# Performance work log

Hardware: AMD Instinct MI355X
Metric: run time of the kernel (lower is better)

## Reference

```python
import jax, jax.numpy as jnp
import numpy as np

NV, NC, E, H, L = 100_000, 420_000, 630_000, 128, 8
ALPHA, THETA = 0.1, 0.5


def _seg_mean(msgs, dst, n_dst):
    # mean aggregation over destination segments (PyG SAGEConv default)
    s = jax.ops.segment_sum(msgs, dst, num_segments=n_dst)
    cnt = jax.ops.segment_sum(jnp.ones((dst.shape[0], 1), msgs.dtype), dst, num_segments=n_dst)
    return s / jnp.maximum(cnt, 1.0)


def _sage(x_src, x_dst, src, dst, n_dst, Wl, bl, Wr):
    # SAGEConv: lin_l(mean_{j in N(i)} x_j) + lin_r(x_i); lin_r has no bias
    agg = _seg_mean(x_src[src], dst, n_dst)
    return agg @ Wl + bl + x_dst @ Wr


def setup_inputs() -> dict:
    key = jax.random.key(0)
    ks = jax.random.split(key, 40)
    k = iter(range(40))
    rn = lambda shape, s=0.05: jax.random.normal(ks[next(k)], shape, jnp.float32) * s
    inp = {}
    inp['x_variable'] = jax.random.normal(ks[next(k)], (NV, 4), jnp.float32)
    inp['x_clause'] = jax.random.normal(ks[next(k)], (NC, 1), jnp.float32)
    src_p = jax.random.randint(ks[next(k)], (E,), 0, NV)
    dst_p = jax.random.randint(ks[next(k)], (E,), 0, NC)
    src_n = jax.random.randint(ks[next(k)], (E,), 0, NV)
    dst_n = jax.random.randint(ks[next(k)], (E,), 0, NC)
    inp['edge_pos'] = jnp.stack([src_p, dst_p])  # variable -> clause
    inp['edge_neg'] = jnp.stack([src_n, dst_n])
    inp['W_vemb'] = rn((4, H)); inp['b_vemb'] = rn((H,))
    inp['W_cemb'] = rn((1, H)); inp['b_cemb'] = rn((H,))
    for tag in ('pos', 'neg', 'rpos', 'rneg'):
        inp[f'Wl_{tag}'] = rn((L, H, H)); inp[f'bl_{tag}'] = rn((L, H))
        inp[f'Wr_{tag}'] = rn((L, H, H))
    inp['Wv'] = rn((L, H, H)); inp['bv'] = rn((L, H))
    inp['W_fin'] = rn((H, 1)); inp['b_fin'] = rn((1,))
    return inp


def reference(x_variable, x_clause, edge_pos, edge_neg,
              W_vemb, b_vemb, W_cemb, b_cemb,
              Wl_pos, bl_pos, Wr_pos, Wl_neg, bl_neg, Wr_neg,
              Wl_rpos, bl_rpos, Wr_rpos, Wl_rneg, bl_rneg, Wr_rneg,
              Wv, bv, W_fin, b_fin):
    v_h0 = jax.nn.relu(x_variable @ W_vemb + b_vemb)
    c_h0 = jax.nn.relu(x_clause @ W_cemb + b_cemb)
    v_h, c_h = v_h0, c_h0
    sp, dp = edge_pos[0], edge_pos[1]
    sn, dn = edge_neg[0], edge_neg[1]
    for i in range(L):
        v_old = v_h
        # HeteroConv(aggr='sum'): clause gets pos_in + neg_in, variable gets rev_pos_in + rev_neg_in
        c_new = (_sage(v_h, c_h, sp, dp, NC, Wl_pos[i], bl_pos[i], Wr_pos[i]) +
                 _sage(v_h, c_h, sn, dn, NC, Wl_neg[i], bl_neg[i], Wr_neg[i]))
        v_new = (_sage(c_h, v_h, dp, sp, NV, Wl_rpos[i], bl_rpos[i], Wr_rpos[i]) +
                 _sage(c_h, v_h, dn, sn, NV, Wl_rneg[i], bl_rneg[i], Wr_rneg[i]))
        v_h = (1.0 - ALPHA) * v_new + ALPHA * v_h0
        c_h = (1.0 - ALPHA) * c_new + ALPHA * c_h0
        beta = float(np.log(THETA / (i + 1) + 1.0))
        v_h = (1.0 - beta) * v_h + beta * (v_h @ Wv[i] + bv[i])
        v_h = v_h + v_old  # use_inter_layer_res=True
        v_h, c_h = jax.nn.relu(v_h), jax.nn.relu(c_h)
    return v_h @ W_fin + b_fin
```

## Files before the change

kernel.cpp:

```cpp
#include <hip/hip_runtime.h>
#include <math.h>

#define NVV 100000
#define NCC 420000
#define EE  630000
#define HH  128
#define LL  8

typedef unsigned int uint;
typedef unsigned short ushort;
typedef __attribute__((ext_vector_type(8))) short bf16x8;
typedef __attribute__((ext_vector_type(4))) float f32x4;

#define MFMA16(a,b,c) __builtin_amdgcn_mfma_f32_16x16x32_bf16(a,b,c,0,0,0)
#define SW(r,k) (((r)<<7) + ((k) ^ (((r)&7)<<3)))

__device__ inline float bf2f(uint u){ return __uint_as_float(u << 16); }
__device__ inline uint  f2bf(float f){
  uint b = __float_as_uint(f);
  return (b + 0x7FFFu + ((b >> 16) & 1u)) >> 16;
}
__device__ inline uint pack2(float a, float b){ return f2bf(a) | (f2bf(b) << 16); }
__device__ inline float4 relu4(float4 v){
  v.x = fmaxf(v.x, 0.f); v.y = fmaxf(v.y, 0.f);
  v.z = fmaxf(v.z, 0.f); v.w = fmaxf(v.w, 0.f);
  return v;
}

__global__ void k_sentinel(float* out, float v){
  if (blockIdx.x == 0 && threadIdx.x == 0) out[0] = v;
}

__device__ inline float4 vemb4(const float* __restrict__ xv, const float* __restrict__ W,
                               const float* __restrict__ b, int i, int h4){
  float x0 = xv[4*i+0], x1 = xv[4*i+1], x2 = xv[4*i+2], x3 = xv[4*i+3];
  float4 w0 = *(const float4*)(W + 0*HH + h4);
  float4 w1 = *(const float4*)(W + 1*HH + h4);
  float4 w2 = *(const float4*)(W + 2*HH + h4);
  float4 w3 = *(const float4*)(W + 3*HH + h4);
  float4 bb = *(const float4*)(b + h4);
  float4 r;
  r.x = fmaf(x0,w0.x, fmaf(x1,w1.x, fmaf(x2,w2.x, fmaf(x3,w3.x, bb.x))));
  r.y = fmaf(x0,w0.y, fmaf(x1,w1.y, fmaf(x2,w2.y, fmaf(x3,w3.y, bb.y))));
  r.z = fmaf(x0,w0.z, fmaf(x1,w1.z, fmaf(x2,w2.z, fmaf(x3,w3.z, bb.z))));
  r.w = fmaf(x0,w0.w, fmaf(x1,w1.w, fmaf(x2,w2.w, fmaf(x3,w3.w, bb.w))));
  return r;
}

__global__ void k_embed_v(const float* __restrict__ xv, const float* __restrict__ W,
                          const float* __restrict__ b, float* __restrict__ out){
  int tid = blockIdx.x * 256 + threadIdx.x;
  int i = tid >> 5;
  if (i >= NVV) return;
  int h4 = (tid & 31) << 2;
  *(float4*)(out + (size_t)i*HH + h4) = relu4(vemb4(xv, W, b, i, h4));
}

__global__ void k_embed_c(const float* __restrict__ xc, const float* __restrict__ W,
                          const float* __restrict__ b, uint* __restrict__ out){
  int tid = blockIdx.x * 256 + threadIdx.x;
  int i = tid >> 5;
  if (i >= NCC) return;
  int c2 = tid & 31;
  int h4 = c2 << 2;
  float x0 = xc[i];
  float4 w = *(const float4*)(W + h4);
  float4 bb = *(const float4*)(b + h4);
  float4 r;
  r.x = fmaxf(fmaf(x0, w.x, bb.x), 0.f);
  r.y = fmaxf(fmaf(x0, w.y, bb.y), 0.f);
  r.z = fmaxf(fmaf(x0, w.z, bb.z), 0.f);
  r.w = fmaxf(fmaf(x0, w.w, bb.w), 0.f);
  uint2 o; o.x = pack2(r.x, r.y); o.y = pack2(r.z, r.w);
  *(uint2*)(out + (size_t)i*64 + c2*2) = o;
}

__global__ void k_prep(const float* __restrict__ Wl_pos, const float* __restrict__ Wl_neg,
                       const float* __restrict__ Wl_rpos, const float* __restrict__ Wl_rneg,
                       const float* __restrict__ Wv, const float* __restrict__ Wr_pos,
                       const float* __restrict__ Wr_neg, const float* __restrict__ Wr_rpos,
                       const float* __restrict__ Wr_rneg, ushort* __restrict__ wt){
  int tid = blockIdx.x * 256 + threadIdx.x;
  int n4 = tid & 31, k = (tid >> 5) & 127, l = (tid >> 12) & 7, m = tid >> 15;
  const float* s1; const float* s2 = nullptr;
  switch (m){
    case 0: s1 = Wl_pos;  break;
    case 1: s1 = Wl_neg;  break;
    case 2: s1 = Wl_rpos; break;
    case 3: s1 = Wl_rneg; break;
    case 4: s1 = Wv;      break;
    case 5: s1 = Wr_pos;  s2 = Wr_neg;  break;
    default: s1 = Wr_rpos; s2 = Wr_rneg; break;
  }
  size_t o = (size_t)l*16384 + (size_t)k*128 + n4*4;
  float4 w = *(const float4*)(s1 + o);
  if (s2){
    float4 w2 = *(const float4*)(s2 + o);
    w.x += w2.x; w.y += w2.y; w.z += w2.z; w.w += w2.w;
  }
  ushort* hi = wt + (size_t)((m*LL + l)*2    )*16384;
  ushort* lo = wt + (size_t)((m*LL + l)*2 + 1)*16384;
  float vv[4] = {w.x, w.y, w.z, w.w};
  #pragma unroll
  for (int e = 0; e < 4; ++e){
    int n = n4*4 + e;
    uint h = f2bf(vv[e]);
    float r = vv[e] - bf2f(h);
    hi[SW(n, k)] = (ushort)h;
    lo[SW(n, k)] = (ushort)f2bf(r);
  }
}

__global__ void k_counti(const int* __restrict__ d, int* cnt, int n){
  int i = blockIdx.x * 256 + threadIdx.x;
  if (i < n) atomicAdd(&cnt[d[i]], 1);
}

#define SCAN256(ts, t) \
  for (int off = 1; off < 256; off <<= 1){ \
    int _a = (t >= off) ? ts[t - off] : 0; \
    __syncthreads(); \
    ts[t] += _a; \
    __syncthreads(); \
  }

__global__ void k_scanb(const int* __restrict__ in, int* __restrict__ out,
                        int* __restrict__ part, int n){
  __shared__ int ts[256];
  int b = blockIdx.x, t = threadIdx.x;
  int base = b*1024 + t*4;
  int v0 = (base+0 < n) ? in[base+0] : 0;
  int v1 = (base+1 < n) ? in[base+1] : 0;
  int v2 = (base+2 < n) ? in[base+2] : 0;
  int v3 = (base+3 < n) ? in[base+3] : 0;
  int s1 = v0, s2 = s1+v1, s3 = s2+v2, tsum = s3+v3;
  ts[t] = tsum; __syncthreads();
  SCAN256(ts, t)
  int excl = ts[t] - tsum;
  if (base+0 < n) out[base+0] = excl;
  if (base+1 < n) out[base+1] = excl + s1;
  if (base+2 < n) out[base+2] = excl + s2;
  if (base+3 < n) out[base+3] = excl + s3;
  if (t == 255) part[b] = ts[255];
}

__global__ void k_scanp(int* p, int nb){
  __shared__ int ts[256];
  __shared__ int carry;
  int t = threadIdx.x;
  if (t == 0) carry = 0;
  __syncthreads();
  for (int c = 0; c*256 < nb; ++c){
    int i = c*256 + t;
    int v = (i < nb) ? p[i] : 0;
    ts[t] = v; __syncthreads();
    SCAN256(ts, t)
    int excl = ts[t] - v + carry;
    if (i < nb) p[i] = excl;
    int tot = ts[255];
    __syncthreads();
    if (t == 0) carry += tot;
    __syncthreads();
  }
}

__global__ void k_scana(int* out, const int* __restrict__ part, int n){
  int i = blockIdx.x * 256 + threadIdx.x;
  if (i < n) out[i] += part[i >> 10];
}

__global__ void k_fill(const int* __restrict__ dst, const int* __restrict__ pay,
                       int* cur, int* __restrict__ eo, int n){
  int i = blockIdx.x * 256 + threadIdx.x;
  if (i >= n) return;
  int p = atomicAdd(&cur[dst[i]], 1);
  eo[p] = pay[i];
}

__global__ void k_vgather(const uint* __restrict__ ch,
                          const int* __restrict__ ipp, const int* __restrict__ epp,
                          const int* __restrict__ ipn, const int* __restrict__ epn,
                          uint* __restrict__ Up, uint* __restrict__ Un){
  int g = blockIdx.x * 256 + threadIdx.x;
  int v = g >> 6, lane = g & 63;
  if (v >= NVV) return;
  int sp = v ? ipp[v-1] : 0, ePos = ipp[v];
  int sn = v ? ipn[v-1] : 0, eNeg = ipn[v];
  float p0 = 0.f, p1 = 0.f, n0 = 0.f, n1 = 0.f;
  int jp = sp, jn = sn;
  while (jp < ePos && jn < eNeg){
    uint up = ch[(size_t)epp[jp]*64 + lane];
    uint un = ch[(size_t)epn[jn]*64 + lane];
    p0 += bf2f(up & 0xFFFFu); p1 += bf2f(up >> 16);
    n0 += bf2f(un & 0xFFFFu); n1 += bf2f(un >> 16);
    ++jp; ++jn;
  }
  for (; jp < ePos; ++jp){
    uint up = ch[(size_t)epp[jp]*64 + lane];
    p0 += bf2f(up & 0xFFFFu); p1 += bf2f(up >> 16);
  }
  for (; jn < eNeg; ++jn){
    uint un = ch[(size_t)epn[jn]*64 + lane];
    n0 += bf2f(un & 0xFFFFu); n1 += bf2f(un >> 16);
  }
  float ivp = 1.f / fmaxf((float)(ePos - sp), 1.f);
  float ivn = 1.f / fmaxf((float)(eNeg - sn), 1.f);
  Up[(size_t)v*64 + lane] = pack2(p0*ivp, p1*ivp);
  Un[(size_t)v*64 + lane] = pack2(n0*ivn, n1*ivn);
}

__device__ inline void stA_bf16(const uint4* __restrict__ A, ushort* As, int m0, int M, int t){
  #pragma unroll
  for (int j = 0; j < 4; ++j){
    int idx = j*512 + t, r = idx >> 4, c = idx & 15;
    uint4 v = make_uint4(0,0,0,0);
    if (m0 + r < M) v = A[(size_t)(m0 + r)*16 + c];
    *(uint4*)(As + SW(r, c*8)) = v;
  }
}

__device__ inline void stA_f32(const float* __restrict__ A, ushort* As, int m0, int M, int t){
  const float4* A4 = (const float4*)A;
  #pragma unroll
  for (int j = 0; j < 8; ++j){
    int idx = j*512 + t, r = idx >> 5, c = idx & 31;
    float4 v = make_float4(0.f,0.f,0.f,0.f);
    if (m0 + r < M) v = A4[(size_t)(m0 + r)*32 + c];
    uint2 u; u.x = pack2(v.x, v.y); u.y = pack2(v.z, v.w);
    *(uint2*)(As + SW(r, c*4)) = u;
  }
}

__device__ inline void stB(const uint4* __restrict__ Bt, ushort* Bs, int t){
  #pragma unroll
  for (int j = 0; j < 4; ++j) ((uint4*)Bs)[j*512 + t] = Bt[j*512 + t];
}

__device__ inline void stB64(const uint4* __restrict__ Bt, ushort* Bs64, int khalf, int t){
  #pragma unroll
  for (int j = 0; j < 2; ++j){
    int idx = j*512 + t;
    int n = idx >> 3, c = idx & 7;
    ((uint4*)Bs64)[n*8 + c] = Bt[n*16 + khalf*8 + c];
  }
}

__device__ inline void kloop(const ushort* As, const ushort* Bs, int wr, int wc,
                             int l15, int g, f32x4 acc[2][4]){
  #pragma unroll
  for (int kk = 0; kk < 4; ++kk){
    int kb = kk*32 + g*8;
    bf16x8 a0 = *(const bf16x8*)(As + SW(wr*32 + l15,      kb));
    bf16x8 a1 = *(const bf16x8*)(As + SW(wr*32 + 16 + l15, kb));
    #pragma unroll
    for (int ni = 0; ni < 4; ++ni){
      int n = wc*64 + ni*16 + l15;
      bf16x8 b = *(const bf16x8*)(Bs + SW(n, kb));
      acc[0][ni] = MFMA16(a0, b, acc[0][ni]);
      acc[1][ni] = MFMA16(a1, b, acc[1][ni]);
    }
  }
}

__device__ inline void kloop64(const ushort* As, const ushort* Bs64, int kbase,
                               int wr, int wc, int l15, int g, f32x4 acc[2][4]){
  #pragma unroll
  for (int kk = 0; kk < 2; ++kk){
    int kb = kk*32 + g*8;
    bf16x8 a0 = *(const bf16x8*)(As + SW(wr*32 + l15,      kbase + kb));
    bf16x8 a1 = *(const bf16x8*)(As + SW(wr*32 + 16 + l15, kbase + kb));
    #pragma unroll
    for (int ni = 0; ni < 4; ++ni){
      int n = wc*64 + ni*16 + l15;
      bf16x8 b = *(const bf16x8*)(Bs64 + ((n<<6) + (kb ^ ((n&7)<<3))));
      acc[0][ni] = MFMA16(a0, b, acc[0][ni]);
      acc[1][ni] = MFMA16(a1, b, acc[1][ni]);
    }
  }
}

__device__ inline void accStoreF(float* ldsF, f32x4 acc[2][4], int wr, int wc, int l15, int g){
  #pragma unroll
  for (int mi = 0; mi < 2; ++mi)
    #pragma unroll
    for (int ni = 0; ni < 4; ++ni)
      #pragma unroll
      for (int j = 0; j < 4; ++j)
        ldsF[(wr*32 + mi*16 + g*4 + j)*128 + wc*64 + ni*16 + l15] = acc[mi][ni][j];
}

__device__ inline void accStoreBf(ushort* dst, f32x4 acc[2][4], int wr, int wc, int l15, int g){
  #pragma unroll
  for (int mi = 0; mi < 2; ++mi)
    #pragma unroll
    for (int ni = 0; ni < 4; ++ni)
      #pragma unroll
      for (int j = 0; j < 4; ++j)
        dst[(wr*32 + mi*16 + g*4 + j)*128 + wc*64 + ni*16 + l15] =
            (ushort)f2bf(acc[mi][ni][j]);
}

#define MMHEAD \
  __shared__ ushort lds[32768]; \
  ushort* As = lds; ushort* Bs = lds + 16384; \
  float* accumF = (float*)lds; \
  int t = threadIdx.x, m0 = blockIdx.x * 128; \
  int w = t >> 6, l = t & 63, wr = w >> 1, wc = w & 1, l15 = l & 15, g = l >> 4; \
  const f32x4 zz = {0.f, 0.f, 0.f, 0.f}; \
  (void)accumF;

#define ZACC(A) { \
  _Pragma("unroll") for (int mi_ = 0; mi_ < 2; ++mi_) \
    _Pragma("unroll") for (int ni_ = 0; ni_ < 4; ++ni_) A[mi_][ni_] = zz; }

__global__ __launch_bounds__(512) void k_fused_v(
    const uint4* __restrict__ AggP, const uint4* __restrict__ AggN,
    const uint4* __restrict__ Bph, const uint4* __restrict__ Bpl,
    const uint4* __restrict__ Bnh, const uint4* __restrict__ Bnl,
    const uint4* __restrict__ Bfh, const uint4* __restrict__ Bfl,
    const uint4* __restrict__ Byph, const uint4* __restrict__ Bypl,
    const uint4* __restrict__ Bynh, const uint4* __restrict__ Bynl,
    const uint4* __restrict__ Bvh, const uint4* __restrict__ Bvl,
    const float* __restrict__ xv, const float* __restrict__ Wve, const float* __restrict__ bve,
    const float* __restrict__ blp, const float* __restrict__ bln, const float* __restrict__ bvv,
    float omb, float beta,
    uint4* __restrict__ Yp, uint4* __restrict__ Yn, float* vh, int M){
  MMHEAD
  f32x4 accM[2][4], accP[2][4], accN[2][4];
  ZACC(accM) ZACC(accP) ZACC(accN)

  stA_bf16(AggP, As, m0, M, t); stB(Bph, Bs, t); __syncthreads();
  kloop(As, Bs, wr, wc, l15, g, accM); __syncthreads();
  stB(Bpl, Bs, t); __syncthreads();
  kloop(As, Bs, wr, wc, l15, g, accM); __syncthreads();
  stA_bf16(AggN, As, m0, M, t); stB(Bnh, Bs, t); __syncthreads();
  kloop(As, Bs, wr, wc, l15, g, accM); __syncthreads();
  stB(Bnl, Bs, t); __syncthreads();
  kloop(As, Bs, wr, wc, l15, g, accM); __syncthreads();
  stA_f32(vh, As, m0, M, t); stB(Bfh, Bs, t); __syncthreads();
  kloop(As, Bs, wr, wc, l15, g, accM); __syncthreads();
  stB(Bfl, Bs, t); __syncthreads();
  kloop(As, Bs, wr, wc, l15, g, accM); __syncthreads();
  stB(Byph, Bs, t); __syncthreads();
  kloop(As, Bs, wr, wc, l15, g, accP); __syncthreads();
  stB(Bypl, Bs, t); __syncthreads();
  kloop(As, Bs, wr, wc, l15, g, accP); __syncthreads();
  stB(Bynh, Bs, t); __syncthreads();
  kloop(As, Bs, wr, wc, l15, g, accN); __syncthreads();
  stB(Bynl, Bs, t); __syncthreads();
  kloop(As, Bs, wr, wc, l15, g, accN);

  __syncthreads();
  accStoreBf(lds,         accP, wr, wc, l15, g);
  accStoreBf(lds + 16384, accN, wr, wc, l15, g);
  __syncthreads();
  #pragma unroll
  for (int j = 0; j < 4; ++j){
    int idx = j*512 + t, r = idx >> 4, c = idx & 15;
    if (m0 + r < M){
      Yp[(size_t)(m0 + r)*16 + c] = ((const uint4*)lds)[idx];
      Yn[(size_t)(m0 + r)*16 + c] = ((const uint4*)(lds + 16384))[idx];
    }
  }
  __syncthreads();

  accStoreF(accumF, accM, wr, wc, l15, g);
  __syncthreads();
  float4 vreg[8];
  #pragma unroll
  for (int j = 0; j < 8; ++j){
    int idx = j*512 + t, r = idx >> 5, c4 = idx & 31;
    int row = m0 + r;
    float4 o = make_float4(0.f,0.f,0.f,0.f);
    if (row < M){
      float4 a4 = ((const float4*)accumF)[r*32 + c4];
      float4 bp = ((const float4*)blp)[c4];
      float4 bn = ((const float4*)bln)[c4];
      float4 h = relu4(vemb4(xv, Wve, bve, row, c4*4));
      o.x = 0.9f*(a4.x + bp.x + bn.x) + 0.1f*h.x;
      o.y = 0.9f*(a4.y + bp.y + bn.y) + 0.1f*h.y;
      o.z = 0.9f*(a4.z + bp.z + bn.z) + 0.1f*h.z;
      o.w = 0.9f*(a4.w + bp.w + bn.w) + 0.1f*h.w;
    }
    vreg[j] = o;
  }
  __syncthreads();
  #pragma unroll
  for (int j = 0; j < 8; ++j){
    int idx = j*512 + t, r = idx >> 5, c4 = idx & 31;
    uint2 u; u.x = pack2(vreg[j].x, vreg[j].y); u.y = pack2(vreg[j].z, vreg[j].w);
    *(uint2*)(As + SW(r, c4*4)) = u;
  }
  f32x4 accT[2][4];
  ZACC(accT)
  stB(Bvh, Bs, t); __syncthreads();
  kloop(As, Bs, wr, wc, l15, g, accT); __syncthreads();
  stB(Bvl, Bs, t); __syncthreads();
  kloop(As, Bs, wr, wc, l15, g, accT);

  float* ldsH = (float*)Bs;
  #pragma unroll
  for (int half = 0; half < 2; ++half){
    __syncthreads();
    if ((wr >> 1) == half){
      int rbase = (wr & 1)*32;
      #pragma unroll
      for (int mi = 0; mi < 2; ++mi)
        #pragma unroll
        for (int ni = 0; ni < 4; ++ni)
          #pragma unroll
          for (int j = 0; j < 4; ++j)
            ldsH[(rbase + mi*16 + g*4 + j)*128 + wc*64 + ni*16 + l15] = accT[mi][ni][j];
    }
    __syncthreads();
    #pragma unroll
    for (int j = 0; j < 4; ++j){
      int idx = j*512 + t, r2 = idx >> 5, c4 = idx & 31;
      int row = m0 + half*64 + r2;
      if (row >= M) continue;
      float4 a4 = ((const float4*)ldsH)[r2*32 + c4];
      uint2 um = *(const uint2*)(As + SW(half*64 + r2, c4*4));
      float4 bb = ((const float4*)bvv)[c4];
      float4 vo = *(const float4*)(vh + (size_t)row*HH + c4*4);
      float m0f = bf2f(um.x & 0xFFFFu), m1f = bf2f(um.x >> 16);
      float m2f = bf2f(um.y & 0xFFFFu), m3f = bf2f(um.y >> 16);
      float4 o;
      o.x = fmaxf(omb*m0f + beta*(a4.x + bb.x) + vo.x, 0.f);
      o.y = fmaxf(omb*m1f + beta*(a4.y + bb.y) + vo.y, 0.f);
      o.z = fmaxf(omb*m2f + beta*(a4.z + bb.z) + vo.z, 0.f);
      o.w = fmaxf(omb*m3f + beta*(a4.w + bb.w) + vo.w, 0.f);
      *(float4*)(vh + (size_t)row*HH + c4*4) = o;
    }
  }
}

__device__ inline void addrow8(float f[8], uint4 u){
  f[0] += bf2f(u.x & 0xFFFFu); f[1] += bf2f(u.x >> 16);
  f[2] += bf2f(u.y & 0xFFFFu); f[3] += bf2f(u.y >> 16);
  f[4] += bf2f(u.z & 0xFFFFu); f[5] += bf2f(u.z >> 16);
  f[6] += bf2f(u.w & 0xFFFFu); f[7] += bf2f(u.w >> 16);
}

__global__ __launch_bounds__(512) void k_mm_c(const uint4* ch,
    const uint4* __restrict__ Bh, const uint4* __restrict__ Bl,
    const int* __restrict__ ipp, const int* __restrict__ ecp,
    const int* __restrict__ ipn, const int* __restrict__ ecn,
    const uint4* __restrict__ Yp, const uint4* __restrict__ Yn,
    const float* __restrict__ xc, const float* __restrict__ Wc, const float* __restrict__ bc,
    const float* __restrict__ blp, const float* __restrict__ bln,
    uint4* chout){
  __shared__ ushort lds[24576];
  ushort* As = lds;
  ushort* Bs = lds + 16384;
  int t = threadIdx.x, m0 = blockIdx.x * 128;
  int w = t >> 6, l = t & 63, wr = w >> 1, wc = w & 1, l15 = l & 15, g = l >> 4;
  const f32x4 zz = {0.f, 0.f, 0.f, 0.f};
  f32x4 acc[2][4];
  ZACC(acc)
  stA_bf16(ch, As, m0, NCC, t);
  stB64(Bh, Bs, 0, t); __syncthreads();
  kloop64(As, Bs, 0,  wr, wc, l15, g, acc); __syncthreads();
  stB64(Bh, Bs, 1, t); __syncthreads();
  kloop64(As, Bs, 64, wr, wc, l15, g, acc); __syncthreads();
  stB64(Bl, Bs, 0, t); __syncthreads();
  kloop64(As, Bs, 0,  wr, wc, l15, g, acc); __syncthreads();
  stB64(Bl, Bs, 1, t); __syncthreads();
  kloop64(As, Bs, 64, wr, wc, l15, g, acc);
  __syncthreads();
  accStoreBf(As, acc, wr, wc, l15, g);
  __syncthreads();

  int c16 = t & 15;
  int rg  = t >> 4;
  #pragma unroll
  for (int pass = 0; pass < 4; ++pass){
    int r = pass*32 + rg;
    int row = m0 + r;
    if (row >= NCC) continue;
    float fp[8] = {0,0,0,0,0,0,0,0};
    float fn[8] = {0,0,0,0,0,0,0,0};
    int sp = row ? ipp[row-1] : 0, ePos = ipp[row];
    int sn = row ? ipn[row-1] : 0, eNeg = ipn[row];
    int jp = sp, jn = sn;
    while (jp < ePos && jn < eNeg){
      uint4 up = Yp[(size_t)ecp[jp]*16 + c16];
      uint4 un = Yn[(size_t)ecn[jn]*16 + c16];
      addrow8(fp, up);
      addrow8(fn, un);
      ++jp; ++jn;
    }
    for (; jp < ePos; ++jp) addrow8(fp, Yp[(size_t)ecp[jp]*16 + c16]);
    for (; jn < eNeg; ++jn) addrow8(fn, Yn[(size_t)ecn[jn]*16 + c16]);
    float invp = 1.f / fmaxf((float)(ePos - sp), 1.f);
    float invn = 1.f / fmaxf((float)(eNeg - sn), 1.f);

    uint4 ru = *(const uint4*)(As + r*128 + c16*8);
    float res[8];
    res[0] = bf2f(ru.x & 0xFFFFu); res[1] = bf2f(ru.x >> 16);
    res[2] = bf2f(ru.y & 0xFFFFu); res[3] = bf2f(ru.y >> 16);
    res[4] = bf2f(ru.z & 0xFFFFu); res[5] = bf2f(ru.z >> 16);
    res[6] = bf2f(ru.w & 0xFFFFu); res[7] = bf2f(ru.w >> 16);
    int gi0 = c16*2, gi1 = gi0 + 1;
    float4 wc0 = ((const float4*)Wc)[gi0],  wc1 = ((const float4*)Wc)[gi1];
    float4 bc0 = ((const float4*)bc)[gi0],  bc1 = ((const float4*)bc)[gi1];
    float4 bp0 = ((const float4*)blp)[gi0], bp1 = ((const float4*)blp)[gi1];
    float4 bn0 = ((const float4*)bln)[gi0], bn1 = ((const float4*)bln)[gi1];
    float xcv = xc[row];
    float wcv[8] = {wc0.x,wc0.y,wc0.z,wc0.w, wc1.x,wc1.y,wc1.z,wc1.w};
    float bcv[8] = {bc0.x,bc0.y,bc0.z,bc0.w, bc1.x,bc1.y,bc1.z,bc1.w};
    float bpv[8] = {bp0.x,bp0.y,bp0.z,bp0.w, bp1.x,bp1.y,bp1.z,bp1.w};
    float bnv[8] = {bn0.x,bn0.y,bn0.z,bn0.w, bn1.x,bn1.y,bn1.z,bn1.w};
    float o[8];
    #pragma unroll
    for (int k = 0; k < 8; ++k){
      float h = fmaxf(fmaf(xcv, wcv[k], bcv[k]), 0.f);
      float m = fmaf(fp[k], invp, fn[k]*invn);
      o[k] = fmaxf(0.9f*(m + res[k] + bpv[k] + bnv[k]) + 0.1f*h, 0.f);
    }
    uint4 u;
    u.x = pack2(o[0], o[1]); u.y = pack2(o[2], o[3]);
    u.z = pack2(o[4], o[5]); u.w = pack2(o[6], o[7]);
    chout[(size_t)row*16 + c16] = u;
  }
}

__global__ void k_final(const float* __restrict__ vh, const float* __restrict__ wf,
                        const float* __restrict__ bf, float* __restrict__ out){
  int wid = (blockIdx.x * 256 + threadIdx.x) >> 6;
  if (wid >= NVV) return;
  int lane = threadIdx.x & 63;
  float2 a = *(const float2*)(vh + (size_t)wid*HH + lane*2);
  float2 w = *(const float2*)(wf + lane*2);
  float s = a.x*w.x + a.y*w.y;
  #pragma unroll
  for (int off = 32; off > 0; off >>= 1) s += __shfl_down(s, off);
  if (lane == 0) out[wid] = s + bf[0];
}

extern "C" void kernel_launch(void* const* d_in, const int* in_sizes, int n_in,
                              void* d_out, int out_size, void* d_ws, size_t ws_size,
                              hipStream_t stream) {
  const float* xv  = (const float*)d_in[0];
  const float* xc  = (const float*)d_in[1];
  const int*   ep  = (const int*)d_in[2];
  const int*   en  = (const int*)d_in[3];
  const float* Wve = (const float*)d_in[4];
  const float* bve = (const float*)d_in[5];
  const float* Wce = (const float*)d_in[6];
  const float* bce = (const float*)d_in[7];
  const float* Wl_pos  = (const float*)d_in[8];
  const float* bl_pos  = (const float*)d_in[9];
  const float* Wr_pos  = (const float*)d_in[10];
  const float* Wl_neg  = (const float*)d_in[11];
  const float* bl_neg  = (const float*)d_in[12];
  const float* Wr_neg  = (const float*)d_in[13];
  const float* Wl_rpos = (const float*)d_in[14];
  const float* bl_rpos = (const float*)d_in[15];
  const float* Wr_rpos = (const float*)d_in[16];
  const float* Wl_rneg = (const float*)d_in[17];
  const float* bl_rneg = (const float*)d_in[18];
  const float* Wr_rneg = (const float*)d_in[19];
  const float* Wv  = (const float*)d_in[20];
  const float* bv  = (const float*)d_in[21];
  const float* Wf  = (const float*)d_in[22];
  const float* bf  = (const float*)d_in[23];
  float* out = (float*)d_out;

  size_t off = 0;
  auto alloc = [&](size_t bytes) -> void* {
    void* p = (char*)d_ws + off;
    off = (off + bytes + 255) & ~(size_t)255;
    return p;
  };
  uint*   c_h  = (uint*)  alloc((size_t)NCC*64*sizeof(uint));
  float*  v_h  = (float*) alloc((size_t)NVV*HH*sizeof(float));
  uint*   U1   = (uint*)  alloc((size_t)NVV*64*sizeof(uint));
  uint*   U2   = (uint*)  alloc((size_t)NVV*64*sizeof(uint));
  ushort* wt   = (ushort*)alloc((size_t)7*LL*2*16384*sizeof(ushort));
  int*   ipc_p = (int*)  alloc((size_t)NCC*sizeof(int));
  int*   ec_p  = (int*)  alloc((size_t)EE*sizeof(int));
  int*   ipc_n = (int*)  alloc((size_t)NCC*sizeof(int));
  int*   ec_n  = (int*)  alloc((size_t)EE*sizeof(int));
  int*   ipv_p = (int*)  alloc((size_t)NVV*sizeof(int));
  int*   ev_p  = (int*)  alloc((size_t)EE*sizeof(int));
  int*   ipv_n = (int*)  alloc((size_t)NVV*sizeof(int));
  int*   ev_n  = (int*)  alloc((size_t)EE*sizeof(int));
  int*   part  = (int*)  alloc(4096);
  if (off > ws_size){
    k_sentinel<<<1, 64, 0, stream>>>(out, (float)(ws_size >> 20));
    return;
  }

  const int TB = 256;
  const int gE  = (EE + TB-1)/TB;
  const int gV  = (NVV*32 + TB-1)/TB;
  const int gC  = (NCC*32 + TB-1)/TB;
  const int gGv = (NVV + 127)/128;
  const int gGc = (NCC + 127)/128;
  const int gWd = (NVV*64 + TB-1)/TB;

  auto wp = [&](int m, int l, int h) -> const uint4* {
    return (const uint4*)(wt + (size_t)((m*LL + l)*2 + h)*16384);
  };

  auto build = [&](const int* dst, const int* pay, int nd, int* ip, int* eo){
    hipMemsetAsync(ip, 0, (size_t)nd*sizeof(int), stream);
    k_counti<<<gE, TB, 0, stream>>>(dst, ip, EE);
    int nb = (nd + 1023)/1024;
    k_scanb<<<nb, TB, 0, stream>>>(ip, ip, part, nd);
    k_scanp<<<1, TB, 0, stream>>>(part, nb);
    k_scana<<<(nd + TB-1)/TB, TB, 0, stream>>>(ip, part, nd);
    k_fill<<<gE, TB, 0, stream>>>(dst, pay, ip, eo, EE);
  };
  build(ep + EE, ep,      NCC, ipc_p, ec_p);
  build(en + EE, en,      NCC, ipc_n, ec_n);
  build(ep,      ep + EE, NVV, ipv_p, ev_p);
  build(en,      en + EE, NVV, ipv_n, ev_n);

  k_prep<<<(7*LL*128*32)/TB, TB, 0, stream>>>(Wl_pos, Wl_neg, Wl_rpos, Wl_rneg, Wv,
                                              Wr_pos, Wr_neg, Wr_rpos, Wr_rneg, wt);

  k_embed_v<<<gV, TB, 0, stream>>>(xv, Wve, bve, v_h);
  k_embed_c<<<gC, TB, 0, stream>>>(xc, Wce, bce, c_h);

  for (int l = 0; l < LL; ++l){
    const size_t bo = (size_t)l*HH;
    double beta_d = log(0.5/(double)(l+1) + 1.0);

    k_vgather<<<gWd, TB, 0, stream>>>(c_h, ipv_p, ev_p, ipv_n, ev_n, U1, U2);
    k_fused_v<<<gGv, 512, 0, stream>>>((const uint4*)U1, (const uint4*)U2,
                                       wp(2,l,0), wp(2,l,1), wp(3,l,0), wp(3,l,1),
                                       wp(6,l,0), wp(6,l,1),
                                       wp(0,l,0), wp(0,l,1), wp(1,l,0), wp(1,l,1),
                                       wp(4,l,0), wp(4,l,1),
                                       xv, Wve, bve, bl_rpos + bo, bl_rneg + bo, bv + bo,
                                       (float)(1.0 - beta_d), (float)beta_d,
                                       (uint4*)U1, (uint4*)U2, v_h, NVV);
    k_mm_c<<<gGc, 512, 0, stream>>>((const uint4*)c_h, wp(5,l,0), wp(5,l,1),
                                    ipc_p, ec_p, ipc_n, ec_n,
                                    (const uint4*)U1, (const uint4*)U2,
                                    xc, Wce, bce, bl_pos + bo, bl_neg + bo,
                                    (uint4*)c_h);
  }

  k_final<<<gWd, TB, 0, stream>>>(v_h, Wf, bf, out);
}
```

Measured before the change: 3.456 ms.

## Double-buffer weight tiles in fused variable kernel with register prefetch

Replaces the single 128x128 B tile in LDS with two 64-wide-K half-tile buffers. Each step issues global loads for the next half-tile into registers before running the MFMA k-loop on the current buffer, then writes the registers to the other buffer. This halves the barriers per step and overlaps weight loading with matrix math. It keeps one extra set of prefetch registers live, which raises register pressure, and it changes the barrier pattern around the A-tile reloads.

Result: no change. 3.523 ms (+1.9%).

```diff
diff --git a/kernel.cpp b/kernel.cpp
--- a/kernel.cpp
+++ b/kernel.cpp
@@ -245,6 +245,21 @@
   }
 }
 
+__device__ inline void ldB64(const uint4* __restrict__ Bt, int khalf, uint4 br[2], int t){
+  #pragma unroll
+  for (int j = 0; j < 2; ++j){
+    int idx = j*512 + t, n = idx >> 3, c = idx & 7;
+    br[j] = Bt[n*16 + khalf*8 + c];
+  }
+}
+__device__ inline void wrB64(ushort* Bs64, const uint4 br[2], int t){
+  #pragma unroll
+  for (int j = 0; j < 2; ++j){
+    int idx = j*512 + t, n = idx >> 3, c = idx & 7;
+    ((uint4*)Bs64)[n*8 + c] = br[j];
+  }
+}
+
 __device__ inline void kloop(const ushort* As, const ushort* Bs, int wr, int wc,
                              int l15, int g, f32x4 acc[2][4]){
   #pragma unroll
@@ -300,18 +315,15 @@
             (ushort)f2bf(acc[mi][ni][j]);
 }
 
-#define MMHEAD \
-  __shared__ ushort lds[32768]; \
-  ushort* As = lds; ushort* Bs = lds + 16384; \
-  float* accumF = (float*)lds; \
-  int t = threadIdx.x, m0 = blockIdx.x * 128; \
-  int w = t >> 6, l = t & 63, wr = w >> 1, wc = w & 1, l15 = l & 15, g = l >> 4; \
-  const f32x4 zz = {0.f, 0.f, 0.f, 0.f}; \
-  (void)accumF;
-
 #define ZACC(A) { \
   _Pragma("unroll") for (int mi_ = 0; mi_ < 2; ++mi_) \
     _Pragma("unroll") for (int ni_ = 0; ni_ < 4; ++ni_) A[mi_][ni_] = zz; }
+
+#define HSF(SIDX, ACC, NM, NH) \
+  ldB64(NM, NH, br, t); \
+  kloop64(As, ((SIDX)&1) ? Bs1 : Bs0, ((SIDX)&1)*64, wr, wc, l15, g, ACC); \
+  wrB64((((SIDX)+1)&1) ? Bs1 : Bs0, br, t); \
+  __syncthreads();
 
 __global__ __launch_bounds__(512) void k_fused_v(
     const uint4* __restrict__ AggP, const uint4* __restrict__ AggN,
@@ -325,32 +337,50 @@
     const float* __restrict__ blp, const float* __restrict__ bln, const float* __restrict__ bvv,
     float omb, float beta,
     uint4* __restrict__ Yp, uint4* __restrict__ Yn, float* vh, int M){
-  MMHEAD
+  __shared__ ushort lds[32768];
+  ushort* As  = lds;
+  ushort* Bs0 = lds + 16384;
+  ushort* Bs1 = lds + 24576;
+  float* accumF = (float*)lds;
+  int t = threadIdx.x, m0 = blockIdx.x * 128;
+  int w = t >> 6, l = t & 63, wr = w >> 1, wc = w & 1, l15 = l & 15, g = l >> 4;
+  const f32x4 zz = {0.f, 0.f, 0.f, 0.f};
   f32x4 accM[2][4], accP[2][4], accN[2][4];
   ZACC(accM) ZACC(accP) ZACC(accN)
-
-  stA_bf16(AggP, As, m0, M, t); stB(Bph, Bs, t); __syncthreads();
-  kloop(As, Bs, wr, wc, l15, g, accM); __syncthreads();
-  stB(Bpl, Bs, t); __syncthreads();
-  kloop(As, Bs, wr, wc, l15, g, accM); __syncthreads();
-  stA_bf16(AggN, As, m0, M, t); stB(Bnh, Bs, t); __syncthreads();
-  kloop(As, Bs, wr, wc, l15, g, accM); __syncthreads();
-  stB(Bnl, Bs, t); __syncthreads();
-  kloop(As, Bs, wr, wc, l15, g, accM); __syncthreads();
-  stA_f32(vh, As, m0, M, t); stB(Bfh, Bs, t); __syncthreads();
-  kloop(As, Bs, wr, wc, l15, g, accM); __syncthreads();
-  stB(Bfl, Bs, t); __syncthreads();
-  kloop(As, Bs, wr, wc, l15, g, accM); __syncthreads();
-  stB(Byph, Bs, t); __syncthreads();
-  kloop(As, Bs, wr, wc, l15, g, accP); __syncthreads();
-  stB(Bypl, Bs, t); __syncthreads();
-  kloop(As, Bs, wr, wc, l15, g, accP); __syncthreads();
-  stB(Bynh, Bs, t); __syncthreads();
-  kloop(As, Bs, wr, wc, l15, g, accN); __syncthreads();
-  stB(Bynl, Bs, t); __syncthreads();
-  kloop(As, Bs, wr, wc, l15, g, accN);
-
-  __syncthreads();
+  uint4 br[2], brv[2];
+
+  ldB64(Bph, 0, br, t);
+  stA_bf16(AggP, As, m0, M, t);
+  wrB64(Bs0, br, t);
+  __syncthreads();
+
+  HSF(0, accM, Bph, 1)
+  HSF(1, accM, Bpl, 0)
+  HSF(2, accM, Bpl, 1)
+  HSF(3, accM, Bnh, 0)
+  stA_bf16(AggN, As, m0, M, t);
+  __syncthreads();
+  HSF(4, accM, Bnh, 1)
+  HSF(5, accM, Bnl, 0)
+  HSF(6, accM, Bnl, 1)
+  HSF(7, accM, Bfh, 0)
+  stA_f32(vh, As, m0, M, t);
+  __syncthreads();
+  HSF(8,  accM, Bfh, 1)
+  HSF(9,  accM, Bfl, 0)
+  HSF(10, accM, Bfl, 1)
+  HSF(11, accM, Byph, 0)
+  HSF(12, accP, Byph, 1)
+  HSF(13, accP, Bypl, 0)
+  HSF(14, accP, Bypl, 1)
+  HSF(15, accP, Bynh, 0)
+  HSF(16, accN, Bynh, 1)
+  HSF(17, accN, Bynl, 0)
+  HSF(18, accN, Bynl, 1)
+  ldB64(Bvh, 0, brv, t);
+  kloop64(As, Bs1, 64, wr, wc, l15, g, accN);
+  __syncthreads();
+
   accStoreBf(lds,         accP, wr, wc, l15, g);
   accStoreBf(lds + 16384, accN, wr, wc, l15, g);
   __syncthreads();
@@ -391,14 +421,25 @@
     uint2 u; u.x = pack2(vreg[j].x, vreg[j].y); u.y = pack2(vreg[j].z, vreg[j].w);
     *(uint2*)(As + SW(r, c4*4)) = u;
   }
+  wrB64(Bs0, brv, t);
+  __syncthreads();
   f32x4 accT[2][4];
   ZACC(accT)
-  stB(Bvh, Bs, t); __syncthreads();
-  kloop(As, Bs, wr, wc, l15, g, accT); __syncthreads();
-  stB(Bvl, Bs, t); __syncthreads();
-  kloop(As, Bs, wr, wc, l15, g, accT);
-
-  float* ldsH = (float*)Bs;
+  ldB64(Bvh, 1, brv, t);
+  kloop64(As, Bs0, 0, wr, wc, l15, g, accT);
+  wrB64(Bs1, brv, t);
+  __syncthreads();
+  ldB64(Bvl, 0, brv, t);
+  kloop64(As, Bs1, 64, wr, wc, l15, g, accT);
+  wrB64(Bs0, brv, t);
+  __syncthreads();
+  ldB64(Bvl, 1, brv, t);
+  kloop64(As, Bs0, 0, wr, wc, l15, g, accT);
+  wrB64(Bs1, brv, t);
+  __syncthreads();
+  kloop64(As, Bs1, 64, wr, wc, l15, g, accT);
+
+  float* ldsH = (float*)Bs0;
   #pragma unroll
   for (int half = 0; half < 2; ++half){
     __syncthreads();
```
